# Kernel optimization log

Measured on AMD Instinct MI355X. Metric: run time of the kernel, lower is better.

## Reference

```python
import jax, jax.numpy as jnp
import numpy as np

N_NODES = 100000
N_EDGES = 3200000
D_IN = 512
D_OUT = 256


def setup_inputs() -> dict:
    key = jax.random.key(0)
    k1, k2, k3, k4, k5 = jax.random.split(key, 5)
    x = jax.random.normal(k1, (N_NODES, D_IN), dtype=jnp.float32)
    edge_row = jax.random.randint(k2, (N_EDGES,), 0, N_NODES, dtype=jnp.int32)
    edge_col = jax.random.randint(k3, (N_EDGES,), 0, N_NODES, dtype=jnp.int32)
    edge_vals = jax.random.uniform(k4, (N_EDGES,), dtype=jnp.float32)
    # glorot uniform for W, zeros for bias (as in the torch module)
    init_range = float(np.sqrt(6.0 / (D_IN + D_OUT)))
    W = jax.random.uniform(k5, (D_IN, D_OUT), minval=-init_range, maxval=init_range, dtype=jnp.float32)
    b = jnp.zeros((D_OUT,), dtype=jnp.float32)
    return {"x": x, "edge_row": edge_row, "edge_col": edge_col,
            "edge_vals": edge_vals, "W": W, "b": b}


def reference(x, edge_row, edge_col, edge_vals, W, b):
    # dropout p=0 -> identity; feature transform
    pre_sup = x @ W                                   # [N, D_OUT]
    # SpMM: out[i] = sum_{e: row[e]==i} vals[e] * pre_sup[col[e]]
    gathered = pre_sup[edge_col] * edge_vals[:, None]  # [E, D_OUT]
    agg = jax.ops.segment_sum(gathered, edge_row, num_segments=N_NODES)
    out = agg + b
    # F.normalize(p=2, dim=0): L2-normalize each column over the node dim
    col_norm = jnp.sqrt(jnp.sum(out * out, axis=0, keepdims=True))
    out = out / jnp.maximum(col_norm, 1e-12)
    return jax.nn.softplus(out)
```

## Files before the change

### kernel.cpp

```cpp
#include <hip/hip_runtime.h>
#include <math.h>

#define N_NODES 100000
#define N_EDGES 3200000
#define D_IN 512
#define D_OUT 256
#define NBUK 391
#define LDA 40

typedef unsigned short ushort_t;
typedef unsigned int uint_t;

using f32x4 = __attribute__((ext_vector_type(4))) float;
using s16x8 = __attribute__((ext_vector_type(8))) short;
using u32x4 = __attribute__((ext_vector_type(4))) uint_t;

__device__ __forceinline__ ushort_t f2bf(float f) {
    union { float f; uint_t u; } v; v.f = f;
    uint_t r = v.u + 0x7FFFu + ((v.u >> 16) & 1u);
    return (ushort_t)(r >> 16);
}
__device__ __forceinline__ float bf2f(uint_t u) {
    union { uint_t u; float f; } v; v.u = u << 16;
    return v.f;
}

__global__ __launch_bounds__(256) void cvt_w(const float* __restrict__ W,
                                             ushort_t* __restrict__ Wt) {
    int idx = blockIdx.x * 256 + threadIdx.x;
    int k = idx >> 8, n = idx & 255;
    Wt[(size_t)n * D_IN + k] = f2bf(W[idx]);
}

__global__ __launch_bounds__(256) void gemm_xw(const float* __restrict__ X,
                                               const ushort_t* __restrict__ Wt,
                                               ushort_t* __restrict__ P) {
    __shared__ ushort_t As[128 * LDA];
    __shared__ ushort_t Bs[128 * LDA];
    const int tid = threadIdx.x;
    const int n0 = blockIdx.x * 128;
    const int m0 = blockIdx.y * 128;
    const int wave = tid >> 6, lane = tid & 63;
    const int quad = lane >> 4, r16 = lane & 15;
    const int wm = (wave >> 1) * 64, wn = (wave & 1) * 64;

    f32x4 acc[4][4] = {};

    for (int k0 = 0; k0 < D_IN; k0 += 32) {
#pragma unroll
        for (int it = 0; it < 2; ++it) {
            int f = tid + it * 256;
            int row = f >> 2, kc = (f & 3) * 8;
            int grow = m0 + row;
            s16x8 av = {};
            if (grow < N_NODES) {
                const float* xp = X + (size_t)grow * D_IN + k0 + kc;
                f32x4 v0 = *(const f32x4*)(xp);
                f32x4 v1 = *(const f32x4*)(xp + 4);
                av[0] = (short)f2bf(v0[0]); av[1] = (short)f2bf(v0[1]);
                av[2] = (short)f2bf(v0[2]); av[3] = (short)f2bf(v0[3]);
                av[4] = (short)f2bf(v1[0]); av[5] = (short)f2bf(v1[1]);
                av[6] = (short)f2bf(v1[2]); av[7] = (short)f2bf(v1[3]);
            }
            *(s16x8*)(&As[row * LDA + kc]) = av;
            s16x8 bv = *(const s16x8*)(Wt + (size_t)(n0 + row) * D_IN + k0 + kc);
            *(s16x8*)(&Bs[row * LDA + kc]) = bv;
        }
        __syncthreads();

        s16x8 a[4], b[4];
#pragma unroll
        for (int i = 0; i < 4; ++i)
            a[i] = *(const s16x8*)(&As[(wm + i * 16 + r16) * LDA + quad * 8]);
#pragma unroll
        for (int j = 0; j < 4; ++j)
            b[j] = *(const s16x8*)(&Bs[(wn + j * 16 + r16) * LDA + quad * 8]);
#pragma unroll
        for (int i = 0; i < 4; ++i)
#pragma unroll
            for (int j = 0; j < 4; ++j)
                acc[i][j] = __builtin_amdgcn_mfma_f32_16x16x32_bf16(a[i], b[j], acc[i][j], 0, 0, 0);
        __syncthreads();
    }

#pragma unroll
    for (int i = 0; i < 4; ++i) {
#pragma unroll
        for (int rr = 0; rr < 4; ++rr) {
            int grow = m0 + wm + i * 16 + quad * 4 + rr;
            if (grow >= N_NODES) continue;
#pragma unroll
            for (int j = 0; j < 4; ++j) {
                int gcol = n0 + wn + j * 16 + r16;
                P[(size_t)grow * D_OUT + gcol] = f2bf(acc[i][j][rr]);
            }
        }
    }
}

__global__ __launch_bounds__(256) void bhist(const int* __restrict__ erow,
                                             int* __restrict__ bcnt) {
    __shared__ int l[NBUK];
    for (int b = threadIdx.x; b < NBUK; b += 256) l[b] = 0;
    __syncthreads();
    int base = blockIdx.x * 4096;
#pragma unroll
    for (int i = 0; i < 16; ++i) {
        int e = base + i * 256 + threadIdx.x;
        if (e < N_EDGES) atomicAdd(&l[erow[e] >> 8], 1);
    }
    __syncthreads();
    for (int b = threadIdx.x; b < NBUK; b += 256)
        if (l[b]) atomicAdd(&bcnt[b], l[b]);
}

__global__ void bscan(const int* __restrict__ bcnt, int* __restrict__ bbase,
                      int* __restrict__ bcursor, int* __restrict__ rstart) {
    __shared__ int sc[512];
    int t = threadIdx.x;
    int v = (t < NBUK) ? bcnt[t] : 0;
    sc[t] = v;
    __syncthreads();
    for (int off = 1; off < 512; off <<= 1) {
        int x = (t >= off) ? sc[t - off] : 0;
        __syncthreads();
        sc[t] += x;
        __syncthreads();
    }
    if (t < NBUK) { int excl = sc[t] - v; bbase[t] = excl; bcursor[t] = excl; }
    if (t == 0) { bbase[NBUK] = N_EDGES; rstart[N_NODES] = N_EDGES; }
}

__global__ __launch_bounds__(256) void bucket_scatter(const int* __restrict__ erow,
                                                      const int* __restrict__ ecol,
                                                      const float* __restrict__ eval,
                                                      int* __restrict__ bcursor,
                                                      uint2* __restrict__ bkt) {
    __shared__ int lcnt[NBUK];
    __shared__ int lbase[NBUK];
    const int t = threadIdx.x;
    for (int b = t; b < NBUK; b += 256) lcnt[b] = 0;
    __syncthreads();
    const int base = blockIdx.x * 4096;
#pragma unroll
    for (int i = 0; i < 16; ++i) {
        int e = base + i * 256 + t;
        if (e < N_EDGES) atomicAdd(&lcnt[erow[e] >> 8], 1);
    }
    __syncthreads();
    for (int b = t; b < NBUK; b += 256) {
        int c = lcnt[b];
        if (c) lbase[b] = atomicAdd(&bcursor[b], c);
        lcnt[b] = 0;
    }
    __syncthreads();
#pragma unroll
    for (int i = 0; i < 16; ++i) {
        int e = base + i * 256 + t;
        if (e < N_EDGES) {
            int r = erow[e];
            int b = r >> 8;
            int off = atomicAdd(&lcnt[b], 1);
            uint2 p;
            p.x = ((uint_t)(r & 255) << 17) | (uint_t)ecol[e];
            p.y = __float_as_uint(eval[e]);
            bkt[lbase[b] + off] = p;
        }
    }
}

__global__ __launch_bounds__(256) void csr_build(const uint2* __restrict__ bkt,
                                                 const int* __restrict__ bbase,
                                                 int* __restrict__ rstart,
                                                 uint2* __restrict__ csr) {
    __shared__ int hcnt[256];
    __shared__ int sc[256];
    __shared__ int cur[256];
    const int t = threadIdx.x, b = blockIdx.x;
    const int beg = bbase[b], end = bbase[b + 1];
    hcnt[t] = 0;
    __syncthreads();
    for (int i = beg + t; i < end; i += 256)
        atomicAdd(&hcnt[bkt[i].x >> 17], 1);
    __syncthreads();
    int v = hcnt[t];
    sc[t] = v;
    __syncthreads();
    for (int off = 1; off < 256; off <<= 1) {
        int x = (t >= off) ? sc[t - off] : 0;
        __syncthreads();
        sc[t] += x;
        __syncthreads();
    }
    int excl = sc[t] - v;
    int row = b * 256 + t;
    if (row < N_NODES) rstart[row] = beg + excl;
    cur[t] = excl;
    __syncthreads();
    for (int i = beg + t; i < end; i += 256) {
        uint2 u = bkt[i];
        int lr = u.x >> 17;
        int off = atomicAdd(&cur[lr], 1);
        uint2 o;
        o.x = u.x & 0x1FFFFu;
        o.y = u.y;
        csr[beg + off] = o;
    }
}

__global__ __launch_bounds__(256) void spmm_kernel(const uint2* __restrict__ csr,
                                                   const int* __restrict__ row_start,
                                                   const ushort_t* __restrict__ pre,
                                                   const float* __restrict__ bias,
                                                   float* __restrict__ out) {
    __shared__ uint2 epairs[4][64];
    const int wv   = threadIdx.x >> 6;
    const int lane = threadIdx.x & 63;
    const int half = lane >> 5;
    const int l32  = lane & 31;
    const int node = blockIdx.x * 4 + wv;

    const int beg = row_start[node], end = row_start[node + 1];

    float a0 = 0.f, a1 = 0.f, a2 = 0.f, a3 = 0.f;
    float a4 = 0.f, a5 = 0.f, a6 = 0.f, a7 = 0.f;

    for (int base = beg; base < end; base += 64) {
        const int cnt = min(end - base, 64);
        uint2 p0;
        p0.x = 0u; p0.y = 0u;
        if (lane < cnt) p0 = csr[base + lane];
        epairs[wv][lane] = p0;

        const int iters = (cnt + 7) >> 3;
        for (int it = 0; it < iters; ++it) {
            const int e0 = it * 8 + half;
            uint2 q0 = epairs[wv][e0 + 0];
            uint2 q1 = epairs[wv][e0 + 2];
            uint2 q2 = epairs[wv][e0 + 4];
            uint2 q3 = epairs[wv][e0 + 6];

            u32x4 g0 = *(const u32x4*)(pre + (((size_t)q0.x) << 8) + l32 * 8);
            u32x4 g1 = *(const u32x4*)(pre + (((size_t)q1.x) << 8) + l32 * 8);
            u32x4 g2 = *(const u32x4*)(pre + (((size_t)q2.x) << 8) + l32 * 8);
            u32x4 g3 = *(const u32x4*)(pre + (((size_t)q3.x) << 8) + l32 * 8);

            const float w0 = __uint_as_float(q0.y);
            const float w1 = __uint_as_float(q1.y);
            const float w2 = __uint_as_float(q2.y);
            const float w3 = __uint_as_float(q3.y);

            a0 = fmaf(w0, bf2f(g0[0] & 0xFFFFu), a0);
            a1 = fmaf(w0, bf2f(g0[0] >> 16),     a1);
            a2 = fmaf(w0, bf2f(g0[1] & 0xFFFFu), a2);
            a3 = fmaf(w0, bf2f(g0[1] >> 16),     a3);
            a4 = fmaf(w0, bf2f(g0[2] & 0xFFFFu), a4);
            a5 = fmaf(w0, bf2f(g0[2] >> 16),     a5);
            a6 = fmaf(w0, bf2f(g0[3] & 0xFFFFu), a6);
            a7 = fmaf(w0, bf2f(g0[3] >> 16),     a7);

            a0 = fmaf(w1, bf2f(g1[0] & 0xFFFFu), a0);
            a1 = fmaf(w1, bf2f(g1[0] >> 16),     a1);
            a2 = fmaf(w1, bf2f(g1[1] & 0xFFFFu), a2);
            a3 = fmaf(w1, bf2f(g1[1] >> 16),     a3);
            a4 = fmaf(w1, bf2f(g1[2] & 0xFFFFu), a4);
            a5 = fmaf(w1, bf2f(g1[2] >> 16),     a5);
            a6 = fmaf(w1, bf2f(g1[3] & 0xFFFFu), a6);
            a7 = fmaf(w1, bf2f(g1[3] >> 16),     a7);

            a0 = fmaf(w2, bf2f(g2[0] & 0xFFFFu), a0);
            a1 = fmaf(w2, bf2f(g2[0] >> 16),     a1);
            a2 = fmaf(w2, bf2f(g2[1] & 0xFFFFu), a2);
            a3 = fmaf(w2, bf2f(g2[1] >> 16),     a3);
            a4 = fmaf(w2, bf2f(g2[2] & 0xFFFFu), a4);
            a5 = fmaf(w2, bf2f(g2[2] >> 16),     a5);
            a6 = fmaf(w2, bf2f(g2[3] & 0xFFFFu), a6);
            a7 = fmaf(w2, bf2f(g2[3] >> 16),     a7);

            a0 = fmaf(w3, bf2f(g3[0] & 0xFFFFu), a0);
            a1 = fmaf(w3, bf2f(g3[0] >> 16),     a1);
            a2 = fmaf(w3, bf2f(g3[1] & 0xFFFFu), a2);
            a3 = fmaf(w3, bf2f(g3[1] >> 16),     a3);
            a4 = fmaf(w3, bf2f(g3[2] & 0xFFFFu), a4);
            a5 = fmaf(w3, bf2f(g3[2] >> 16),     a5);
            a6 = fmaf(w3, bf2f(g3[3] & 0xFFFFu), a6);
            a7 = fmaf(w3, bf2f(g3[3] >> 16),     a7);
        }
    }

    a0 += __shfl_xor(a0, 32);
    a1 += __shfl_xor(a1, 32);
    a2 += __shfl_xor(a2, 32);
    a3 += __shfl_xor(a3, 32);
    a4 += __shfl_xor(a4, 32);
    a5 += __shfl_xor(a5, 32);
    a6 += __shfl_xor(a6, 32);
    a7 += __shfl_xor(a7, 32);

    const int fbase = l32 * 8 + half * 4;
    const float* bp = bias + fbase;
    float s0 = half ? a4 : a0;
    float s1 = half ? a5 : a1;
    float s2 = half ? a6 : a2;
    float s3 = half ? a7 : a3;
    f32x4 o;
    o[0] = s0 + bp[0]; o[1] = s1 + bp[1]; o[2] = s2 + bp[2]; o[3] = s3 + bp[3];
    *(f32x4*)(out + (size_t)node * D_OUT + fbase) = o;
}

__global__ __launch_bounds__(256) void colsq_kernel(const float* __restrict__ out,
                                                    float* __restrict__ colsq) {
    const int f = threadIdx.x;
    float s = 0.f;
    for (int i = blockIdx.x; i < N_NODES; i += gridDim.x) {
        float v = out[(size_t)i * D_OUT + f];
        s = fmaf(v, v, s);
    }
    atomicAdd(&colsq[f], s);
}

__global__ __launch_bounds__(256) void finalize_kernel(float* __restrict__ out,
                                                       const float* __restrict__ colsq) {
    __shared__ float inv[256];
    const int t = threadIdx.x;
    float n = sqrtf(colsq[t]);
    inv[t] = 1.0f / fmaxf(n, 1e-12f);
    __syncthreads();
    const size_t total4 = (size_t)N_NODES * D_OUT / 4;
    for (size_t i = (size_t)blockIdx.x * 256 + t; i < total4; i += (size_t)gridDim.x * 256) {
        f32x4 v = ((const f32x4*)out)[i];
        int fbase = (int)((i * 4) & (D_OUT - 1));
        f32x4 o;
#pragma unroll
        for (int c = 0; c < 4; ++c) {
            float x = v[c] * inv[fbase + c];
            float tt = __expf(x);
            float y = __logf(1.0f + tt);
            o[c] = (x > 20.f) ? x : y;
        }
        ((f32x4*)out)[i] = o;
    }
}

extern "C" void kernel_launch(void* const* d_in, const int* in_sizes, int n_in,
                              void* d_out, int out_size, void* d_ws, size_t ws_size,
                              hipStream_t stream) {
    const float* x    = (const float*)d_in[0];
    const int*   erow = (const int*)d_in[1];
    const int*   ecol = (const int*)d_in[2];
    const float* eval = (const float*)d_in[3];
    const float* W    = (const float*)d_in[4];
    const float* b    = (const float*)d_in[5];
    float* out = (float*)d_out;
    char* ws = (char*)d_ws;

    uint2*    bkt     = (uint2*)   (ws + 0);
    ushort_t* pre     = (ushort_t*)(ws + 0);
    uint2*    csr     = (uint2*)   (ws + 51200000);
    int*      rstart  = (int*)     (ws + 76800000);
    float*    colsq   = (float*)   (ws + 77200016);
    int*      bcnt    = (int*)     (ws + 77201040);
    int*      bbase   = (int*)     (ws + 77202608);
    int*      bcursor = (int*)     (ws + 77204176);
    ushort_t* Wt      = (ushort_t*)(ws + 77205760);

    (void)hipMemsetAsync(bcnt, 0, NBUK * sizeof(int), stream);
    (void)hipMemsetAsync(colsq, 0, D_OUT * sizeof(float), stream);

    bhist<<<782, 256, 0, stream>>>(erow, bcnt);
    bscan<<<1, 512, 0, stream>>>(bcnt, bbase, bcursor, rstart);
    bucket_scatter<<<782, 256, 0, stream>>>(erow, ecol, eval, bcursor, bkt);
    csr_build<<<NBUK, 256, 0, stream>>>(bkt, bbase, rstart, csr);
    cvt_w<<<512, 256, 0, stream>>>(W, Wt);
    gemm_xw<<<dim3(2, 782), 256, 0, stream>>>(x, Wt, pre);
    spmm_kernel<<<N_NODES / 4, 256, 0, stream>>>(csr, rstart, pre, b, out);
    colsq_kernel<<<512, 256, 0, stream>>>(out, colsq);
    finalize_kernel<<<1024, 256, 0, stream>>>(out, colsq);
}
```

Before: 869.2 us.

## Fuse column-norm reduction into SpMM and loop both N tiles per GEMM block

Removes the separate colsq kernel by accumulating squared outputs into shared memory inside the SpMM kernel, then atomically adding them into 8 replicated global column sums that finalize adds together. The GEMM now launches one block per 128-row M tile and loops over both 128-column N tiles. Grid size halves, but X is still re-read from global for each N tile. The fusion avoids one full pass over the 100MB output but adds shared atomics, an extra barrier and global atomics in every SpMM block.

```diff
diff --git a/kernel.cpp b/kernel.cpp
--- a/kernel.cpp
+++ b/kernel.cpp
@@ -7,6 +7,7 @@
 #define D_OUT 256
 #define NBUK 391
 #define LDA 40
+#define NREP 8
 
 typedef unsigned short ushort_t;
 typedef unsigned int uint_t;
@@ -38,61 +39,63 @@
     __shared__ ushort_t As[128 * LDA];
     __shared__ ushort_t Bs[128 * LDA];
     const int tid = threadIdx.x;
-    const int n0 = blockIdx.x * 128;
     const int m0 = blockIdx.y * 128;
     const int wave = tid >> 6, lane = tid & 63;
     const int quad = lane >> 4, r16 = lane & 15;
     const int wm = (wave >> 1) * 64, wn = (wave & 1) * 64;
 
-    f32x4 acc[4][4] = {};
-
-    for (int k0 = 0; k0 < D_IN; k0 += 32) {
-#pragma unroll
-        for (int it = 0; it < 2; ++it) {
-            int f = tid + it * 256;
-            int row = f >> 2, kc = (f & 3) * 8;
-            int grow = m0 + row;
-            s16x8 av = {};
-            if (grow < N_NODES) {
-                const float* xp = X + (size_t)grow * D_IN + k0 + kc;
-                f32x4 v0 = *(const f32x4*)(xp);
-                f32x4 v1 = *(const f32x4*)(xp + 4);
-                av[0] = (short)f2bf(v0[0]); av[1] = (short)f2bf(v0[1]);
-                av[2] = (short)f2bf(v0[2]); av[3] = (short)f2bf(v0[3]);
-                av[4] = (short)f2bf(v1[0]); av[5] = (short)f2bf(v1[1]);
-                av[6] = (short)f2bf(v1[2]); av[7] = (short)f2bf(v1[3]);
+    for (int nt = 0; nt < 2; ++nt) {
+        const int n0 = nt * 128;
+        f32x4 acc[4][4] = {};
+
+        for (int k0 = 0; k0 < D_IN; k0 += 32) {
+#pragma unroll
+            for (int it = 0; it < 2; ++it) {
+                int f = tid + it * 256;
+                int row = f >> 2, kc = (f & 3) * 8;
+                int grow = m0 + row;
+                s16x8 av = {};
+                if (grow < N_NODES) {
+                    const float* xp = X + (size_t)grow * D_IN + k0 + kc;
+                    f32x4 v0 = *(const f32x4*)(xp);
+                    f32x4 v1 = *(const f32x4*)(xp + 4);
+                    av[0] = (short)f2bf(v0[0]); av[1] = (short)f2bf(v0[1]);
+                    av[2] = (short)f2bf(v0[2]); av[3] = (short)f2bf(v0[3]);
+                    av[4] = (short)f2bf(v1[0]); av[5] = (short)f2bf(v1[1]);
+                    av[6] = (short)f2bf(v1[2]); av[7] = (short)f2bf(v1[3]);
+                }
+                *(s16x8*)(&As[row * LDA + kc]) = av;
+                s16x8 bv = *(const s16x8*)(Wt + (size_t)(n0 + row) * D_IN + k0 + kc);
+                *(s16x8*)(&Bs[row * LDA + kc]) = bv;
             }
-            *(s16x8*)(&As[row * LDA + kc]) = av;
-            s16x8 bv = *(const s16x8*)(Wt + (size_t)(n0 + row) * D_IN + k0 + kc);
-            *(s16x8*)(&Bs[row * LDA + kc]) = bv;
-        }
-        __syncthreads();
-
-        s16x8 a[4], b[4];
-#pragma unroll
-        for (int i = 0; i < 4; ++i)
-            a[i] = *(const s16x8*)(&As[(wm + i * 16 + r16) * LDA + quad * 8]);
-#pragma unroll
-        for (int j = 0; j < 4; ++j)
-            b[j] = *(const s16x8*)(&Bs[(wn + j * 16 + r16) * LDA + quad * 8]);
-#pragma unroll
-        for (int i = 0; i < 4; ++i)
+            __syncthreads();
+
+            s16x8 a[4], b[4];
+#pragma unroll
+            for (int i = 0; i < 4; ++i)
+                a[i] = *(const s16x8*)(&As[(wm + i * 16 + r16) * LDA + quad * 8]);
 #pragma unroll
             for (int j = 0; j < 4; ++j)
-                acc[i][j] = __builtin_amdgcn_mfma_f32_16x16x32_bf16(a[i], b[j], acc[i][j], 0, 0, 0);
-        __syncthreads();
-    }
-
-#pragma unroll
-    for (int i = 0; i < 4; ++i) {
-#pragma unroll
-        for (int rr = 0; rr < 4; ++rr) {
-            int grow = m0 + wm + i * 16 + quad * 4 + rr;
-            if (grow >= N_NODES) continue;
-#pragma unroll
-            for (int j = 0; j < 4; ++j) {
-                int gcol = n0 + wn + j * 16 + r16;
-                P[(size_t)grow * D_OUT + gcol] = f2bf(acc[i][j][rr]);
+                b[j] = *(const s16x8*)(&Bs[(wn + j * 16 + r16) * LDA + quad * 8]);
+#pragma unroll
+            for (int i = 0; i < 4; ++i)
+#pragma unroll
+                for (int j = 0; j < 4; ++j)
+                    acc[i][j] = __builtin_amdgcn_mfma_f32_16x16x32_bf16(a[i], b[j], acc[i][j], 0, 0, 0);
+            __syncthreads();
+        }
+
+#pragma unroll
+        for (int i = 0; i < 4; ++i) {
+#pragma unroll
+            for (int rr = 0; rr < 4; ++rr) {
+                int grow = m0 + wm + i * 16 + quad * 4 + rr;
+                if (grow >= N_NODES) continue;
+#pragma unroll
+                for (int j = 0; j < 4; ++j) {
+                    int gcol = n0 + wn + j * 16 + r16;
+                    P[(size_t)grow * D_OUT + gcol] = f2bf(acc[i][j][rr]);
+                }
             }
         }
     }
@@ -212,13 +215,18 @@
                                                    const int* __restrict__ row_start,
                                                    const ushort_t* __restrict__ pre,
                                                    const float* __restrict__ bias,
-                                                   float* __restrict__ out) {
+                                                   float* __restrict__ out,
+                                                   float* __restrict__ colsq) {
     __shared__ uint2 epairs[4][64];
+    __shared__ float lcq[256];
     const int wv   = threadIdx.x >> 6;
     const int lane = threadIdx.x & 63;
     const int half = lane >> 5;
     const int l32  = lane & 31;
     const int node = blockIdx.x * 4 + wv;
+
+    lcq[threadIdx.x] = 0.f;
+    __syncthreads();
 
     const int beg = row_start[node], end = row_start[node + 1];
 
@@ -306,24 +314,25 @@
     f32x4 o;
     o[0] = s0 + bp[0]; o[1] = s1 + bp[1]; o[2] = s2 + bp[2]; o[3] = s3 + bp[3];
     *(f32x4*)(out + (size_t)node * D_OUT + fbase) = o;
-}
-
-__global__ __launch_bounds__(256) void colsq_kernel(const float* __restrict__ out,
-                                                    float* __restrict__ colsq) {
-    const int f = threadIdx.x;
-    float s = 0.f;
-    for (int i = blockIdx.x; i < N_NODES; i += gridDim.x) {
-        float v = out[(size_t)i * D_OUT + f];
-        s = fmaf(v, v, s);
-    }
-    atomicAdd(&colsq[f], s);
+
+    atomicAdd(&lcq[fbase + 0], o[0] * o[0]);
+    atomicAdd(&lcq[fbase + 1], o[1] * o[1]);
+    atomicAdd(&lcq[fbase + 2], o[2] * o[2]);
+    atomicAdd(&lcq[fbase + 3], o[3] * o[3]);
+    __syncthreads();
+    float c = lcq[threadIdx.x];
+    if (c != 0.f)
+        atomicAdd(&colsq[(blockIdx.x & (NREP - 1)) * 256 + threadIdx.x], c);
 }
 
 __global__ __launch_bounds__(256) void finalize_kernel(float* __restrict__ out,
                                                        const float* __restrict__ colsq) {
     __shared__ float inv[256];
     const int t = threadIdx.x;
-    float n = sqrtf(colsq[t]);
+    float s = 0.f;
+#pragma unroll
+    for (int r = 0; r < NREP; ++r) s += colsq[r * 256 + t];
+    float n = sqrtf(s);
     inv[t] = 1.0f / fmaxf(n, 1e-12f);
     __syncthreads();
     const size_t total4 = (size_t)N_NODES * D_OUT / 4;
@@ -359,21 +368,20 @@
     uint2*    csr     = (uint2*)   (ws + 51200000);
     int*      rstart  = (int*)     (ws + 76800000);
     float*    colsq   = (float*)   (ws + 77200016);
-    int*      bcnt    = (int*)     (ws + 77201040);
-    int*      bbase   = (int*)     (ws + 77202608);
-    int*      bcursor = (int*)     (ws + 77204176);
-    ushort_t* Wt      = (ushort_t*)(ws + 77205760);
+    int*      bcnt    = (int*)     (ws + 77208208);
+    int*      bbase   = (int*)     (ws + 77209776);
+    int*      bcursor = (int*)     (ws + 77211344);
+    ushort_t* Wt      = (ushort_t*)(ws + 77212928);
 
     (void)hipMemsetAsync(bcnt, 0, NBUK * sizeof(int), stream);
-    (void)hipMemsetAsync(colsq, 0, D_OUT * sizeof(float), stream);
+    (void)hipMemsetAsync(colsq, 0, NREP * D_OUT * sizeof(float), stream);
 
     bhist<<<782, 256, 0, stream>>>(erow, bcnt);
     bscan<<<1, 512, 0, stream>>>(bcnt, bbase, bcursor, rstart);
     bucket_scatter<<<782, 256, 0, stream>>>(erow, ecol, eval, bcursor, bkt);
     csr_build<<<NBUK, 256, 0, stream>>>(bkt, bbase, rstart, csr);
     cvt_w<<<512, 256, 0, stream>>>(W, Wt);
-    gemm_xw<<<dim3(2, 782), 256, 0, stream>>>(x, Wt, pre);
-    spmm_kernel<<<N_NODES / 4, 256, 0, stream>>>(csr, rstart, pre, b, out);
-    colsq_kernel<<<512, 256, 0, stream>>>(out, colsq);
+    gemm_xw<<<dim3(1, 782), 256, 0, stream>>>(x, Wt, pre);
+    spmm_kernel<<<N_NODES / 4, 256, 0, stream>>>(csr, rstart, pre, b, out, colsq);
     finalize_kernel<<<1024, 256, 0, stream>>>(out, colsq);
 }
```

Result: faster. 845.3 us (-2.8%).
